# Performance work log

Hardware: AMD Instinct MI355X
Metric: run time of the kernel (lower is better)

Reference implementation:

```python
import jax, jax.numpy as jnp
import numpy as np

BLOCK = 64  # bnb NF4 blocksize

# NF4 quantile codebook (bitsandbytes quant_type='nf4')
NF4_CODEBOOK = jnp.array([
    -1.0, -0.6961928009986877, -0.5250730514526367, -0.39491748809814453,
    -0.28444138169288635, -0.18477343022823334, -0.09105003625154495, 0.0,
    0.07958029955625534, 0.16093020141124725, 0.24611230194568634,
    0.33791524171829224, 0.44070982933044434, 0.5626170039176941,
    0.7229568362236023, 1.0], dtype=jnp.float32)

IN_FEATURES = 4096
OUT_FEATURES = 11008


def setup_inputs() -> dict:
    key = jax.random.key(0)
    k1, k2, k3 = jax.random.split(key, 3)
    x = jax.random.normal(k1, (4, 2048, IN_FEATURES), dtype=jnp.float32)
    codes = jax.random.randint(k2, (OUT_FEATURES, IN_FEATURES), 0, 16, dtype=jnp.int32)
    n_blocks = OUT_FEATURES * IN_FEATURES // BLOCK
    absmax = jax.random.uniform(k3, (n_blocks,), dtype=jnp.float32)
    return {"x": x, "codes": codes, "absmax": absmax}


def dequant_nf4(codes, absmax):
    # codes: [out, in] int codes in [0,16); absmax: [out*in/BLOCK] per-block scale
    w = NF4_CODEBOOK[codes].reshape(-1, BLOCK)          # [n_blocks, BLOCK]
    w = w * absmax[:, None]                              # blockwise rescale
    return w.reshape(codes.shape)                        # [out, in]


def reference(x, codes, absmax):
    # y = x @ dequant(W)^T  (nn.Linear semantics, bias=False)
    W = dequant_nf4(codes, absmax)                       # [out, in]
    return jnp.einsum('bsi,oi->bso', x, W)
```

## Files before the change

kernel.cpp:

```cpp
#include <hip/hip_runtime.h>
#include <stdint.h>

typedef unsigned short u16;

#define IN_F   4096
#define OUT_F  11008
#define M_TOT  8192

__device__ __constant__ float NF4_TAB[16] = {
    -1.0f, -0.6961928009986877f, -0.5250730514526367f, -0.39491748809814453f,
    -0.28444138169288635f, -0.18477343022823334f, -0.09105003625154495f, 0.0f,
    0.07958029955625534f, 0.16093020141124725f, 0.24611230194568634f,
    0.33791524171829224f, 0.44070982933044434f, 0.5626170039176941f,
    0.7229568362236023f, 1.0f};

static __device__ __forceinline__ unsigned f2bf(float f) {
  unsigned u = __float_as_uint(f);
  u += 0x7fffu + ((u >> 16) & 1u);
  return u >> 16;
}

__global__ __launch_bounds__(256) void dequant_w_kernel(
    const int* __restrict__ codes, const float* __restrict__ absmax,
    uint4* __restrict__ wout, int n8) {
  __shared__ float lut[16];
  if (threadIdx.x < 16) lut[threadIdx.x] = NF4_TAB[threadIdx.x];
  __syncthreads();
  int t = blockIdx.x * 256 + threadIdx.x;
  if (t >= n8) return;
  const int4* cp = (const int4*)codes + (size_t)t * 2;
  int4 c0 = cp[0];
  int4 c1 = cp[1];
  float am = absmax[t >> 3];
  unsigned h0 = f2bf(lut[c0.x] * am) | (f2bf(lut[c0.y] * am) << 16);
  unsigned h1 = f2bf(lut[c0.z] * am) | (f2bf(lut[c0.w] * am) << 16);
  unsigned h2 = f2bf(lut[c1.x] * am) | (f2bf(lut[c1.y] * am) << 16);
  unsigned h3 = f2bf(lut[c1.z] * am) | (f2bf(lut[c1.w] * am) << 16);
  wout[t] = make_uint4(h0, h1, h2, h3);
}

__global__ __launch_bounds__(256) void convert_x_kernel(
    const float4* __restrict__ x, uint4* __restrict__ xout, int n8) {
  int t = blockIdx.x * 256 + threadIdx.x;
  if (t >= n8) return;
  float4 a = x[(size_t)t * 2];
  float4 b = x[(size_t)t * 2 + 1];
  unsigned h0 = f2bf(a.x) | (f2bf(a.y) << 16);
  unsigned h1 = f2bf(a.z) | (f2bf(a.w) << 16);
  unsigned h2 = f2bf(b.x) | (f2bf(b.y) << 16);
  unsigned h3 = f2bf(b.z) | (f2bf(b.w) << 16);
  xout[t] = make_uint4(h0, h1, h2, h3);
}

typedef __attribute__((ext_vector_type(8))) short short8;
typedef __attribute__((ext_vector_type(4))) float f32x4;

static __device__ __forceinline__ void async_copy16(const u16* g, u16* l) {
  __builtin_amdgcn_global_load_lds(
      (const __attribute__((address_space(1))) unsigned int*)g,
      (__attribute__((address_space(3))) unsigned int*)l, 16, 0, 0);
}

__global__ __launch_bounds__(512, 2) void gemm256_bt_bf16_kernel(
    const u16* __restrict__ A,
    const u16* __restrict__ B,
    float* __restrict__ C) {
  constexpr int K  = IN_F;
  constexpr int N  = OUT_F;
  constexpr int NT = K / 64;
  __shared__ u16 lds[2][2][256 * 64];

  const int tid   = threadIdx.x;
  const int wave  = tid >> 6;
  const int lane  = tid & 63;
  const int wr    = wave >> 2;
  const int wc    = wave & 3;
  const int row16 = lane & 15;
  const int quad  = lane >> 4;
  const int swz   = (row16 & 7) << 3;

  const int orig = blockIdx.x;
  const int tile = (orig & 7) * 172 + (orig >> 3);
  const int mb = tile / 43, nb = tile % 43;
  const int m0 = mb * 256, n0 = nb * 256;

  const int sr   = lane >> 3;
  const int scol = ((lane & 7) ^ sr) << 3;
  const u16* ag = A + (size_t)(m0 + wave * 32 + sr) * K + scol;
  const u16* bg = B + (size_t)(n0 + wave * 32 + sr) * K + scol;
  const int ldsbase = wave * 32 * 64;

  f32x4 acc[8][4] = {};

#pragma unroll
  for (int j = 0; j < 4; ++j)
    async_copy16(ag + (size_t)(j * 8) * K, &lds[0][0][ldsbase + j * 512]);
#pragma unroll
  for (int j = 0; j < 4; ++j)
    async_copy16(bg + (size_t)(j * 8) * K, &lds[0][1][ldsbase + j * 512]);

  int cur = 0;
  for (int t = 0; t < NT; ++t) {
    const int tn = (t < NT - 1) ? t + 1 : t;
    {
      u16* An = &lds[cur ^ 1][0][0];
      u16* Bn = &lds[cur ^ 1][1][0];
#pragma unroll
      for (int j = 0; j < 4; ++j)
        async_copy16(ag + (size_t)(j * 8) * K + tn * 64, &An[ldsbase + j * 512]);
#pragma unroll
      for (int j = 0; j < 4; ++j)
        async_copy16(bg + (size_t)(j * 8) * K + tn * 64, &Bn[ldsbase + j * 512]);
    }
    asm volatile("s_waitcnt vmcnt(8)\ns_barrier" ::: "memory");

    const u16* Ac = &lds[cur][0][0];
    const u16* Bc = &lds[cur][1][0];

    short8 bf[4][2];
#pragma unroll
    for (int j = 0; j < 4; ++j)
#pragma unroll
      for (int kx = 0; kx < 2; ++kx)
        bf[j][kx] = *(const short8*)&Bc[(wc * 64 + j * 16 + row16) * 64 +
                                        ((kx * 32 + quad * 8) ^ swz)];

#pragma unroll
    for (int p = 0; p < 4; ++p) {
      if (p) asm volatile("s_barrier" ::: "memory");
      short8 af[2][2];
#pragma unroll
      for (int ii = 0; ii < 2; ++ii)
#pragma unroll
        for (int kx = 0; kx < 2; ++kx)
          af[ii][kx] = *(const short8*)&Ac[(wr * 128 + (p * 2 + ii) * 16 + row16) * 64 +
                                           ((kx * 32 + quad * 8) ^ swz)];
      __builtin_amdgcn_s_setprio(1);
#pragma unroll
      for (int ii = 0; ii < 2; ++ii)
#pragma unroll
        for (int j = 0; j < 4; ++j)
#pragma unroll
          for (int kx = 0; kx < 2; ++kx)
            acc[p * 2 + ii][j] = __builtin_amdgcn_mfma_f32_16x16x32_bf16(
                af[ii][kx], bf[j][kx], acc[p * 2 + ii][j], 0, 0, 0);
      __builtin_amdgcn_s_setprio(0);
    }
    asm volatile("s_barrier" ::: "memory");
    cur ^= 1;
  }
  asm volatile("s_waitcnt vmcnt(0)" ::: "memory");

#pragma unroll
  for (int i = 0; i < 8; ++i)
#pragma unroll
    for (int j = 0; j < 4; ++j)
#pragma unroll
      for (int r = 0; r < 4; ++r)
        C[(size_t)(m0 + wr * 128 + i * 16 + quad * 4 + r) * N +
          (n0 + wc * 64 + j * 16 + row16)] = acc[i][j][r];
}

__global__ void fallback_kernel(const float* __restrict__ x,
                                const int* __restrict__ codes,
                                const float* __restrict__ absmax,
                                float* __restrict__ out) {
  __shared__ float lut[16];
  __shared__ float xs[16][17];
  __shared__ float ws[16][17];
  const int tx = threadIdx.x, ty = threadIdx.y;
  if (ty == 0 && tx < 16) lut[tx] = NF4_TAB[tx];
  __syncthreads();
  const int m  = blockIdx.y * 16 + ty;
  const int n0 = blockIdx.x * 16;
  float acc = 0.f;
  for (int k0 = 0; k0 < IN_F; k0 += 16) {
    xs[ty][tx] = x[(size_t)m * IN_F + k0 + tx];
    int idx = (n0 + ty) * IN_F + k0 + tx;
    ws[ty][tx] = lut[codes[idx]] * absmax[idx >> 6];
    __syncthreads();
#pragma unroll
    for (int kk = 0; kk < 16; ++kk) acc += xs[ty][kk] * ws[tx][kk];
    __syncthreads();
  }
  out[(size_t)m * OUT_F + n0 + tx] = acc;
}

extern "C" void kernel_launch(void* const* d_in, const int* in_sizes, int n_in,
                              void* d_out, int out_size, void* d_ws, size_t ws_size,
                              hipStream_t stream) {
  const float* x      = (const float*)d_in[0];
  const int*   codes  = (const int*)d_in[1];
  const float* absmax = (const float*)d_in[2];
  float* out = (float*)d_out;

  const size_t wBytes = (size_t)OUT_F * IN_F * 2;
  const size_t xBytes = (size_t)M_TOT * IN_F * 2;

  if (ws_size >= wBytes + xBytes) {
    u16* wq = (u16*)d_ws;
    u16* xq = (u16*)((char*)d_ws + wBytes);

    const int n8w = OUT_F * IN_F / 8;
    dequant_w_kernel<<<(n8w + 255) / 256, 256, 0, stream>>>(
        codes, absmax, (uint4*)wq, n8w);

    const int n8x = M_TOT * IN_F / 8;
    convert_x_kernel<<<(n8x + 255) / 256, 256, 0, stream>>>(
        (const float4*)x, (uint4*)xq, n8x);

    const int nwg = (M_TOT / 256) * (OUT_F / 256);
    gemm256_bt_bf16_kernel<<<nwg, 512, 0, stream>>>(xq, wq, out);
  } else {
    dim3 blk(16, 16);
    dim3 grid(OUT_F / 16, M_TOT / 16);
    fallback_kernel<<<grid, blk, 0, stream>>>(x, codes, absmax, out);
  }
}
```

Measured before the change: 1.266 ms.

## Interleave half-tile async LDS loads across MFMA phases with 2x unrolled K loop

Restructures the GEMM main loop into a two-iteration unrolled schedule. Global-to-LDS async copies for A and B are split into half-tile stages and spread across the four MFMA phases, so load issue overlaps compute instead of being issued in one burst per K step. B for the next buffer is prefetched earlier than A. This adds more barriers and tighter vmcnt accounting, which risks extra synchronisation stalls and subtle LDS buffer hazards.

```diff
diff --git a/kernel.cpp b/kernel.cpp
--- a/kernel.cpp
+++ b/kernel.cpp
@@ -61,13 +61,54 @@
       (__attribute__((address_space(3))) unsigned int*)l, 16, 0, 0);
 }
 
+#define STAGE(BUF, AB, HALF, GP, KT)                                         \
+  do {                                                                       \
+    const u16* g_ = (GP) + (size_t)((HALF) * 128) * K + (KT) * 64;           \
+    u16* l_ = &lds[BUF][AB][((HALF) * 128 + wave * 8) * 64];                 \
+    async_copy16(g_, l_);                                                    \
+    async_copy16(g_ + (size_t)64 * K, l_ + 64 * 64);                         \
+  } while (0)
+
+#define PHASE(BUF, P, LOADB, ...)                                            \
+  do {                                                                       \
+    if (LOADB) {                                                             \
+      const u16* Bc_ = &lds[BUF][1][0];                                      \
+      _Pragma("unroll") for (int j = 0; j < 4; ++j)                          \
+          _Pragma("unroll") for (int kx = 0; kx < 2; ++kx)                   \
+              bf[j][kx] = *(const short8*)&Bc_[(wc * 64 + j * 16 + row16) *  \
+                                                   64 +                      \
+                                               ((kx * 32 + quad * 8) ^ swz)];\
+    }                                                                        \
+    short8 af_[2][2];                                                        \
+    {                                                                        \
+      const u16* Ac_ = &lds[BUF][0][0];                                      \
+      _Pragma("unroll") for (int ii = 0; ii < 2; ++ii)                       \
+          _Pragma("unroll") for (int kx = 0; kx < 2; ++kx)                   \
+              af_[ii][kx] = *(const short8*)&Ac_[(wr * 128 +                 \
+                                                  ((P)*2 + ii) * 16 +        \
+                                                  row16) * 64 +              \
+                                                 ((kx * 32 + quad * 8) ^     \
+                                                  swz)];                     \
+    }                                                                        \
+    __VA_ARGS__;                                                             \
+    asm volatile("s_barrier" ::: "memory");                                  \
+    __builtin_amdgcn_s_setprio(1);                                           \
+    _Pragma("unroll") for (int ii = 0; ii < 2; ++ii)                         \
+        _Pragma("unroll") for (int j = 0; j < 4; ++j)                        \
+            _Pragma("unroll") for (int kx = 0; kx < 2; ++kx)                 \
+                acc[(P)*2 + ii][j] = __builtin_amdgcn_mfma_f32_16x16x32_bf16(\
+                    af_[ii][kx], bf[j][kx], acc[(P)*2 + ii][j], 0, 0, 0);    \
+    __builtin_amdgcn_s_setprio(0);                                           \
+  } while (0)
+
 __global__ __launch_bounds__(512, 2) void gemm256_bt_bf16_kernel(
     const u16* __restrict__ A,
     const u16* __restrict__ B,
     float* __restrict__ C) {
-  constexpr int K  = IN_F;
-  constexpr int N  = OUT_F;
-  constexpr int NT = K / 64;
+  constexpr int K   = IN_F;
+  constexpr int N   = OUT_F;
+  constexpr int NT  = K / 64;
+  constexpr int NIT = NT / 2;
   __shared__ u16 lds[2][2][256 * 64];
 
   const int tid   = threadIdx.x;
@@ -84,70 +125,44 @@
   const int mb = tile / 43, nb = tile % 43;
   const int m0 = mb * 256, n0 = nb * 256;
 
-  const int sr   = lane >> 3;
-  const int scol = ((lane & 7) ^ sr) << 3;
-  const u16* ag = A + (size_t)(m0 + wave * 32 + sr) * K + scol;
-  const u16* bg = B + (size_t)(n0 + wave * 32 + sr) * K + scol;
-  const int ldsbase = wave * 32 * 64;
+  const int sr = lane >> 3;
+  const int sc = ((lane & 7) ^ sr) << 3;
+  const u16* agp = A + (size_t)(m0 + wave * 8 + sr) * K + sc;
+  const u16* bgp = B + (size_t)(n0 + wave * 8 + sr) * K + sc;
 
   f32x4 acc[8][4] = {};
-
-#pragma unroll
-  for (int j = 0; j < 4; ++j)
-    async_copy16(ag + (size_t)(j * 8) * K, &lds[0][0][ldsbase + j * 512]);
-#pragma unroll
-  for (int j = 0; j < 4; ++j)
-    async_copy16(bg + (size_t)(j * 8) * K, &lds[0][1][ldsbase + j * 512]);
-
-  int cur = 0;
-  for (int t = 0; t < NT; ++t) {
-    const int tn = (t < NT - 1) ? t + 1 : t;
-    {
-      u16* An = &lds[cur ^ 1][0][0];
-      u16* Bn = &lds[cur ^ 1][1][0];
-#pragma unroll
-      for (int j = 0; j < 4; ++j)
-        async_copy16(ag + (size_t)(j * 8) * K + tn * 64, &An[ldsbase + j * 512]);
-#pragma unroll
-      for (int j = 0; j < 4; ++j)
-        async_copy16(bg + (size_t)(j * 8) * K + tn * 64, &Bn[ldsbase + j * 512]);
-    }
-    asm volatile("s_waitcnt vmcnt(8)\ns_barrier" ::: "memory");
-
-    const u16* Ac = &lds[cur][0][0];
-    const u16* Bc = &lds[cur][1][0];
-
-    short8 bf[4][2];
-#pragma unroll
-    for (int j = 0; j < 4; ++j)
-#pragma unroll
-      for (int kx = 0; kx < 2; ++kx)
-        bf[j][kx] = *(const short8*)&Bc[(wc * 64 + j * 16 + row16) * 64 +
-                                        ((kx * 32 + quad * 8) ^ swz)];
-
-#pragma unroll
-    for (int p = 0; p < 4; ++p) {
-      if (p) asm volatile("s_barrier" ::: "memory");
-      short8 af[2][2];
-#pragma unroll
-      for (int ii = 0; ii < 2; ++ii)
-#pragma unroll
-        for (int kx = 0; kx < 2; ++kx)
-          af[ii][kx] = *(const short8*)&Ac[(wr * 128 + (p * 2 + ii) * 16 + row16) * 64 +
-                                           ((kx * 32 + quad * 8) ^ swz)];
-      __builtin_amdgcn_s_setprio(1);
-#pragma unroll
-      for (int ii = 0; ii < 2; ++ii)
-#pragma unroll
-        for (int j = 0; j < 4; ++j)
-#pragma unroll
-          for (int kx = 0; kx < 2; ++kx)
-            acc[p * 2 + ii][j] = __builtin_amdgcn_mfma_f32_16x16x32_bf16(
-                af[ii][kx], bf[j][kx], acc[p * 2 + ii][j], 0, 0, 0);
-      __builtin_amdgcn_s_setprio(0);
-    }
-    asm volatile("s_barrier" ::: "memory");
-    cur ^= 1;
+  short8 bf[4][2];
+
+  STAGE(0, 0, 0, agp, 0);
+  STAGE(0, 0, 1, agp, 0);
+  STAGE(0, 1, 0, bgp, 0);
+  STAGE(0, 1, 1, bgp, 0);
+  STAGE(1, 1, 0, bgp, 1);
+  STAGE(1, 1, 1, bgp, 1);
+  asm volatile("s_waitcnt vmcnt(4)\n\ts_barrier" ::: "memory");
+
+  for (int j = 0; j < NIT; ++j) {
+    const int kt1 = 2 * j + 1;
+    const int kt2 = (2 * j + 2 < NT) ? 2 * j + 2 : NT - 1;
+    const int kt3 = (2 * j + 3 < NT) ? 2 * j + 3 : NT - 1;
+    PHASE(0, 0, true,  STAGE(1, 0, 0, agp, kt1));
+    asm volatile("s_barrier" ::: "memory");
+    PHASE(0, 1, false, STAGE(1, 0, 1, agp, kt1);
+                       STAGE(0, 1, 0, bgp, kt2));
+    asm volatile("s_barrier" ::: "memory");
+    PHASE(0, 2, false, STAGE(0, 1, 1, bgp, kt2));
+    asm volatile("s_barrier" ::: "memory");
+    PHASE(0, 3, false, ((void)0));
+    asm volatile("s_waitcnt vmcnt(4)\n\ts_barrier" ::: "memory");
+    PHASE(1, 0, true,  STAGE(0, 0, 0, agp, kt2));
+    asm volatile("s_barrier" ::: "memory");
+    PHASE(1, 1, false, STAGE(0, 0, 1, agp, kt2);
+                       STAGE(1, 1, 0, bgp, kt3));
+    asm volatile("s_barrier" ::: "memory");
+    PHASE(1, 2, false, STAGE(1, 1, 1, bgp, kt3));
+    asm volatile("s_barrier" ::: "memory");
+    PHASE(1, 3, false, ((void)0));
+    asm volatile("s_waitcnt vmcnt(4)\n\ts_barrier" ::: "memory");
   }
   asm volatile("s_waitcnt vmcnt(0)" ::: "memory");
 
```

New measurement: 1.173 ms. -7.4%, faster.
